# Optimization experiments

Measured on AMD Instinct MI355X. Metric: run time of the kernel, lower is better.

The kernel has to match this reference:

```python
import jax, jax.numpy as jnp
import numpy as np

N_NODES = 100000
N_EDGES = 3200000
N_FEAT = 128
HIDDEN = 16


def gcn_conv(x, W, b, row, col, ew, n):
    """PyG GCNConv: linear -> add self-loops -> sym deg-norm -> scatter-add -> bias."""
    x = x @ W  # [n, out]
    loop = jnp.arange(n)
    row = jnp.concatenate([row, loop])
    col = jnp.concatenate([col, loop])
    ew = jnp.concatenate([ew, jnp.ones((n,), ew.dtype)])  # self-loop weight 1
    deg = jax.ops.segment_sum(ew, col, num_segments=n)  # in-degree by edge weight
    dinv = jnp.where(deg > 0, jax.lax.rsqrt(deg), 0.0)
    norm = dinv[row] * ew * dinv[col]  # [E+n]
    # gather source features, scale, scatter-add at destinations
    out = jax.ops.segment_sum(x[row] * norm[:, None], col, num_segments=n)
    return out + b


def setup_inputs() -> dict:
    key = jax.random.key(0)
    k = jax.random.split(key, 7)
    x = jax.random.normal(k[0], (N_NODES, N_FEAT), dtype=jnp.float32)
    edge_index = jax.random.randint(k[1], (2, N_EDGES), 0, N_NODES, dtype=jnp.int64)
    edge_weight = jax.random.uniform(k[2], (N_EDGES,), dtype=jnp.float32)
    s1 = 1.0 / np.sqrt(N_FEAT)
    s2 = 1.0 / np.sqrt(HIDDEN)
    W1 = jax.random.uniform(k[3], (N_FEAT, HIDDEN), jnp.float32, -s1, s1)
    b1 = jnp.zeros((HIDDEN,), jnp.float32)
    W2 = jax.random.uniform(k[4], (HIDDEN, 1), jnp.float32, -s2, s2)
    b2 = jnp.zeros((1,), jnp.float32)
    return {"x": x, "edge_index": edge_index, "edge_weight": edge_weight,
            "W1": W1, "b1": b1, "W2": W2, "b2": b2}


def reference(x, edge_index, edge_weight, W1, b1, W2, b2):
    n = x.shape[0]
    row, col = edge_index[0], edge_index[1]
    h = gcn_conv(x, W1, b1, row, col, edge_weight, n)
    h = jax.nn.relu(h)
    h = gcn_conv(h, W2, b2, row, col, edge_weight, n)
    return jax.nn.sigmoid(h)[:, 0].astype(jnp.float32)  # squeeze(1)
```

## Files before the change

### kernel.cpp

```cpp
#include <hip/hip_runtime.h>
#include <math.h>

#define NNODES 100000
#define NEDGES 3200000
#define NF 128
#define NH 16
#define SB 192
#define NSB 521
#define NBLK 512
#define EPB (NEDGES / NBLK)
#define CAP2 6912

__device__ __forceinline__ unsigned bf16rne(float f) {
    unsigned u = __float_as_uint(f);
    return (u + 0x7fffu + ((u >> 16) & 1u)) >> 16;
}

__global__ void k_hist(const int* __restrict__ col, unsigned* __restrict__ ghist) {
    __shared__ unsigned h[NSB];
    int t = threadIdx.x, b = blockIdx.x;
    for (int i = t; i < NSB; i += 256) h[i] = 0u;
    __syncthreads();
    const int2* c2 = (const int2*)(col + b * EPB);
    for (int i = t; i < EPB / 2; i += 256) {
        int2 c = c2[i];
        atomicAdd(&h[(unsigned)c.x / SB], 1u);
        atomicAdd(&h[(unsigned)c.y / SB], 1u);
    }
    __syncthreads();
    for (int i = t; i < NSB; i += 256) ghist[(size_t)b * NSB + i] = h[i];
}

__global__ __launch_bounds__(NBLK) void k_scan1(unsigned* __restrict__ ghist,
                                                unsigned* __restrict__ totals) {
    int k = blockIdx.x, t = threadIdx.x;
    __shared__ unsigned s[NBLK];
    unsigned v = ghist[(size_t)t * NSB + k];
    s[t] = v;
    __syncthreads();
    for (int off = 1; off < NBLK; off <<= 1) {
        unsigned x = (t >= off) ? s[t - off] : 0u;
        __syncthreads();
        s[t] += x;
        __syncthreads();
    }
    ghist[(size_t)t * NSB + k] = s[t] - v;
    if (t == NBLK - 1) totals[k] = s[t];
}

__global__ void k_scan2(const unsigned* __restrict__ totals, unsigned* __restrict__ sbase,
                        unsigned* __restrict__ start) {
    int t = threadIdx.x;
    __shared__ unsigned s[256];
    unsigned v[3];
    unsigned p = 0;
#pragma unroll
    for (int j = 0; j < 3; ++j) {
        int i = t * 3 + j;
        v[j] = (i < NSB) ? totals[i] : 0u;
        p += v[j];
    }
    s[t] = p;
    __syncthreads();
    for (int off = 1; off < 256; off <<= 1) {
        unsigned x = (t >= off) ? s[t - off] : 0u;
        __syncthreads();
        s[t] += x;
        __syncthreads();
    }
    unsigned run = s[t] - p;
#pragma unroll
    for (int j = 0; j < 3; ++j) {
        int i = t * 3 + j;
        if (i < NSB) sbase[i] = run;
        run += v[j];
    }
    if (t == 255) { sbase[NSB] = NEDGES; start[NNODES] = NEDGES; }
}

__global__ __launch_bounds__(256) void k_scatB1(
        const int* __restrict__ row, const int* __restrict__ col,
        const float* __restrict__ ew,
        const unsigned* __restrict__ ghist, const unsigned* __restrict__ sbase,
        uint2* __restrict__ spack) {
    __shared__ uint2 stage[EPB];
    __shared__ unsigned short sbArr[EPB];
    __shared__ unsigned lcnt[NSB];
    __shared__ unsigned gdelta[NSB];
    __shared__ unsigned scn[256];
    int t = threadIdx.x, b = blockIdx.x;
    int e0 = b * EPB;
    for (int i = t; i < NSB; i += 256) lcnt[i] = 0u;
    __syncthreads();
    const int2* c2 = (const int2*)(col + e0);
    for (int i = t; i < EPB / 2; i += 256) {
        int2 c = c2[i];
        atomicAdd(&lcnt[(unsigned)c.x / SB], 1u);
        atomicAdd(&lcnt[(unsigned)c.y / SB], 1u);
    }
    __syncthreads();
    unsigned v[3];
    unsigned p = 0;
#pragma unroll
    for (int j = 0; j < 3; ++j) {
        int i = t * 3 + j;
        v[j] = (i < NSB) ? lcnt[i] : 0u;
        p += v[j];
    }
    scn[t] = p;
    __syncthreads();
    for (int off = 1; off < 256; off <<= 1) {
        unsigned x = (t >= off) ? scn[t - off] : 0u;
        __syncthreads();
        scn[t] += x;
        __syncthreads();
    }
    unsigned run = scn[t] - p;
    __syncthreads();
    unsigned lst[3];
#pragma unroll
    for (int j = 0; j < 3; ++j) {
        int i = t * 3 + j;
        if (i < NSB) {
            lst[j] = run;
            gdelta[i] = sbase[i] + ghist[(size_t)b * NSB + i] - run;
        }
        run += v[j];
    }
    __syncthreads();
#pragma unroll
    for (int j = 0; j < 3; ++j) {
        int i = t * 3 + j;
        if (i < NSB) lcnt[i] = lst[j];
    }
    __syncthreads();
    const int2* r2 = (const int2*)(row + e0);
    const float2* w2 = (const float2*)(ew + e0);
    for (int i = t; i < EPB / 2; i += 256) {
        int2 rr = r2[i];
        int2 cc = c2[i];
        float2 ww = w2[i];
        unsigned sb = (unsigned)cc.x / SB;
        unsigned ln = (unsigned)cc.x - sb * SB;
        unsigned pos = atomicAdd(&lcnt[sb], 1u);
        stage[pos] = make_uint2((unsigned)rr.x | (ln << 17), __float_as_uint(ww.x));
        sbArr[pos] = (unsigned short)sb;
        sb = (unsigned)cc.y / SB;
        ln = (unsigned)cc.y - sb * SB;
        pos = atomicAdd(&lcnt[sb], 1u);
        stage[pos] = make_uint2((unsigned)rr.y | (ln << 17), __float_as_uint(ww.y));
        sbArr[pos] = (unsigned short)sb;
    }
    __syncthreads();
    for (int i = t; i < EPB; i += 256)
        spack[i + gdelta[sbArr[i]]] = stage[i];
}

__global__ __launch_bounds__(512) void k_sortB2(uint2* __restrict__ spack,
                                                const unsigned* __restrict__ sbase,
                                                unsigned* __restrict__ start,
                                                float* __restrict__ dinv) {
    __shared__ uint2 ed[CAP2];
    __shared__ unsigned hist[SB];
    __shared__ float wdeg[SB];
    __shared__ unsigned scn[512];
    int k = blockIdx.x, t = threadIdx.x;
    unsigned e0 = sbase[k], e1 = sbase[k + 1];
    int ne = (int)(e1 - e0);
    if (t < SB) { hist[t] = 0u; wdeg[t] = 0.f; }
    __syncthreads();
    for (int i = t; i < ne; i += 512) {
        uint2 p = spack[e0 + i];
        unsigned ln = p.x >> 17;
        atomicAdd(&hist[ln], 1u);
        atomicAdd(&wdeg[ln], __uint_as_float(p.y));
    }
    __syncthreads();
    unsigned v = (t < SB) ? hist[t] : 0u;
    scn[t] = v;
    __syncthreads();
    for (int off = 1; off < 512; off <<= 1) {
        unsigned x = (t >= off) ? scn[t - off] : 0u;
        __syncthreads();
        scn[t] += x;
        __syncthreads();
    }
    unsigned excl = scn[t] - v;
    int g = k * SB + t;
    if (t < SB && g < NNODES) {
        start[g] = e0 + excl;
        dinv[g] = rsqrtf(wdeg[t] + 1.0f);
    }
    __syncthreads();
    if (t < SB) hist[t] = excl;
    __syncthreads();
    for (int i = t; i < ne; i += 512) {
        uint2 p = spack[e0 + i];
        unsigned ln = p.x >> 17;
        unsigned pos = atomicAdd(&hist[ln], 1u);
        ed[pos] = make_uint2(p.x & 0x1FFFF, p.y);
    }
    __syncthreads();
    for (int i = t; i < ne; i += 512)
        spack[e0 + i] = ed[i];
}

__global__ void k_xw1n(const float* __restrict__ x, const float* __restrict__ W1,
                       const float* __restrict__ dinv, unsigned* __restrict__ xwn) {
    __shared__ float w[NF * NH];
    for (int t = threadIdx.x; t < NF * NH; t += blockDim.x) w[t] = W1[t];
    __syncthreads();
    int i = blockIdx.x * blockDim.x + threadIdx.x;
    if (i >= NNODES) return;
    float acc[NH];
#pragma unroll
    for (int f = 0; f < NH; ++f) acc[f] = 0.f;
    const float4* xr = (const float4*)(x + (long long)i * NF);
#pragma unroll 8
    for (int k4 = 0; k4 < NF / 4; ++k4) {
        float4 v = xr[k4];
        const float* wk = &w[k4 * 4 * NH];
#pragma unroll
        for (int f = 0; f < NH; ++f)
            acc[f] += v.x * wk[f] + v.y * wk[NH + f] + v.z * wk[2 * NH + f] + v.w * wk[3 * NH + f];
    }
    float di = dinv[i];
    unsigned u[8];
#pragma unroll
    for (int j = 0; j < 8; ++j)
        u[j] = bf16rne(acc[2 * j] * di) | (bf16rne(acc[2 * j + 1] * di) << 16);
    uint4* o = (uint4*)(xwn + (size_t)i * 8);
    o[0] = make_uint4(u[0], u[1], u[2], u[3]);
    o[1] = make_uint4(u[4], u[5], u[6], u[7]);
}

__global__ __launch_bounds__(256) void k_edge1z(
        const uint2* __restrict__ spack, const unsigned* __restrict__ start,
        const unsigned* __restrict__ xwn, const float* __restrict__ dinv,
        const float* __restrict__ b1, const float* __restrict__ W2,
        float* __restrict__ zn) {
    int t = threadIdx.x;
    int n = blockIdx.x * 4 + (t >> 6);
    int lane = t & 63;
    int fg = lane & 3, e4 = lane >> 2;
    unsigned e0 = start[n], e1 = start[n + 1];
    float ax = 0.f, ay = 0.f, az = 0.f, aw = 0.f;
    for (unsigned e = e0 + e4; e < e1; e += 48) {
        unsigned ea = e + 16, eb = e + 32;
        uint2 p0 = spack[e];
        uint2 p1 = spack[ea];
        uint2 p2 = spack[eb];
        bool va = ea < e1, vb = eb < e1;
        unsigned r0 = p0.x;
        unsigned r1 = p1.x & 0x1FFFFu; r1 = r1 < NNODES ? r1 : NNODES - 1u;
        unsigned r2 = p2.x & 0x1FFFFu; r2 = r2 < NNODES ? r2 : NNODES - 1u;
        float w0 = __uint_as_float(p0.y);
        float w1 = va ? __uint_as_float(p1.y) : 0.f;
        float w2 = vb ? __uint_as_float(p2.y) : 0.f;
        uint2 q0 = *(const uint2*)(xwn + (size_t)r0 * 8 + fg * 2);
        uint2 q1 = *(const uint2*)(xwn + (size_t)r1 * 8 + fg * 2);
        uint2 q2 = *(const uint2*)(xwn + (size_t)r2 * 8 + fg * 2);
        ax += __uint_as_float(q0.x << 16) * w0 + __uint_as_float(q1.x << 16) * w1
            + __uint_as_float(q2.x << 16) * w2;
        ay += __uint_as_float(q0.x & 0xffff0000u) * w0 + __uint_as_float(q1.x & 0xffff0000u) * w1
            + __uint_as_float(q2.x & 0xffff0000u) * w2;
        az += __uint_as_float(q0.y << 16) * w0 + __uint_as_float(q1.y << 16) * w1
            + __uint_as_float(q2.y << 16) * w2;
        aw += __uint_as_float(q0.y & 0xffff0000u) * w0 + __uint_as_float(q1.y & 0xffff0000u) * w1
            + __uint_as_float(q2.y & 0xffff0000u) * w2;
    }
#pragma unroll
    for (int m = 4; m < 64; m <<= 1) {
        ax += __shfl_xor(ax, m);
        ay += __shfl_xor(ay, m);
        az += __shfl_xor(az, m);
        aw += __shfl_xor(aw, m);
    }
    uint2 qs = *(const uint2*)(xwn + (size_t)n * 8 + fg * 2);
    ax += __uint_as_float(qs.x << 16);
    ay += __uint_as_float(qs.x & 0xffff0000u);
    az += __uint_as_float(qs.y << 16);
    aw += __uint_as_float(qs.y & 0xffff0000u);
    float di = dinv[n];
    float4 b4 = ((const float4*)b1)[fg];
    float4 w4 = ((const float4*)W2)[fg];
    float s = fmaxf(di * ax + b4.x, 0.f) * w4.x
            + fmaxf(di * ay + b4.y, 0.f) * w4.y
            + fmaxf(di * az + b4.z, 0.f) * w4.z
            + fmaxf(di * aw + b4.w, 0.f) * w4.w;
    s += __shfl_xor(s, 1);
    s += __shfl_xor(s, 2);
    if (lane == 0) zn[n] = s * di;
}

__global__ __launch_bounds__(256) void k_edge2out(
        const uint2* __restrict__ spack, const unsigned* __restrict__ start,
        const float* __restrict__ zn, const float* __restrict__ dinv,
        const float* __restrict__ b2, float* __restrict__ out) {
    int t = threadIdx.x;
    int n = blockIdx.x * 4 + (t >> 6);
    int lane = t & 63;
    unsigned e0 = start[n], e1 = start[n + 1];
    float acc = 0.f;
    for (unsigned e = e0 + lane; e < e1; e += 64) {
        uint2 p = spack[e];
        acc += zn[p.x] * __uint_as_float(p.y);
    }
#pragma unroll
    for (int m = 1; m < 64; m <<= 1) acc += __shfl_xor(acc, m);
    if (lane == 0) {
        float di = dinv[n];
        float v = di * acc + di * zn[n] + b2[0];
        out[n] = 1.f / (1.f + expf(-v));
    }
}

extern "C" void kernel_launch(void* const* d_in, const int* in_sizes, int n_in,
                              void* d_out, int out_size, void* d_ws, size_t ws_size,
                              hipStream_t stream) {
    const float* x  = (const float*)d_in[0];
    const int* eidx = (const int*)d_in[1];
    const float* ew = (const float*)d_in[2];
    const float* W1 = (const float*)d_in[3];
    const float* b1 = (const float*)d_in[4];
    const float* W2 = (const float*)d_in[5];
    const float* b2 = (const float*)d_in[6];
    float* out = (float*)d_out;

    const int* row = eidx;
    const int* col = eidx + NEDGES;

    unsigned* ws = (unsigned*)d_ws;
    uint2*    spack  = (uint2*)ws;
    unsigned* xwn    = ws + 6400000;
    float*    dinv   = (float*)(ws + 7200000);
    float*    zn     = (float*)(ws + 7300000);
    unsigned* start  = ws + 7400000;
    unsigned* sbase  = ws + 7500001;
    unsigned* totals = ws + 7500523;
    unsigned* ghist  = ws + 7501044;

    k_hist   <<<NBLK, 256, 0, stream>>>(col, ghist);
    k_scan1  <<<NSB, NBLK, 0, stream>>>(ghist, totals);
    k_scan2  <<<1, 256, 0, stream>>>(totals, sbase, start);
    k_scatB1 <<<NBLK, 256, 0, stream>>>(row, col, ew, ghist, sbase, spack);
    k_sortB2 <<<NSB, 512, 0, stream>>>(spack, sbase, start, dinv);
    k_xw1n   <<<(NNODES + 255) / 256, 256, 0, stream>>>(x, W1, dinv, xwn);
    k_edge1z <<<NNODES / 4, 256, 0, stream>>>(spack, start, xwn, dinv, b1, W2, zn);
    k_edge2out<<<NNODES / 4, 256, 0, stream>>>(spack, start, zn, dinv, b2, out);
}
```

Before: 159.4 us.

## Replace per-node CSR sort with per-superblock LDS atomic accumulation

Drops the second-level sort that built per-node CSR offsets. Instead, each of the 521 superblocks accumulates its destination features with shared-memory float atomics, in both the layer-1 and layer-2 aggregations. The x@W1 matmul is folded into the histogram launch as extra blocks writing fp32 xw, and a separate pass applies dinv and converts to bf16. This saves the sort pass and its LDS staging, but costs 16 shared atomics per edge in layer 1, more contention, and only 521 blocks of parallelism for the edge work.

```diff
diff --git a/kernel.cpp b/kernel.cpp
--- a/kernel.cpp
+++ b/kernel.cpp
@@ -9,26 +9,54 @@
 #define NSB 521
 #define NBLK 512
 #define EPB (NEDGES / NBLK)
-#define CAP2 6912
+#define XWBLK 391
 
 __device__ __forceinline__ unsigned bf16rne(float f) {
     unsigned u = __float_as_uint(f);
     return (u + 0x7fffu + ((u >> 16) & 1u)) >> 16;
 }
-
-__global__ void k_hist(const int* __restrict__ col, unsigned* __restrict__ ghist) {
+__device__ __forceinline__ float bflo(unsigned u) { return __uint_as_float(u << 16); }
+__device__ __forceinline__ float bfhi(unsigned u) { return __uint_as_float(u & 0xffff0000u); }
+
+__global__ void k_histxw(const int* __restrict__ col, unsigned* __restrict__ ghist,
+                         const float* __restrict__ x, const float* __restrict__ W1,
+                         float* __restrict__ xw) {
+    __shared__ float w[NF * NH];
     __shared__ unsigned h[NSB];
     int t = threadIdx.x, b = blockIdx.x;
-    for (int i = t; i < NSB; i += 256) h[i] = 0u;
-    __syncthreads();
-    const int2* c2 = (const int2*)(col + b * EPB);
-    for (int i = t; i < EPB / 2; i += 256) {
-        int2 c = c2[i];
-        atomicAdd(&h[(unsigned)c.x / SB], 1u);
-        atomicAdd(&h[(unsigned)c.y / SB], 1u);
-    }
-    __syncthreads();
-    for (int i = t; i < NSB; i += 256) ghist[(size_t)b * NSB + i] = h[i];
+    if (b < NBLK) {
+        for (int i = t; i < NSB; i += 256) h[i] = 0u;
+        __syncthreads();
+        const int2* c2 = (const int2*)(col + b * EPB);
+        for (int i = t; i < EPB / 2; i += 256) {
+            int2 c = c2[i];
+            atomicAdd(&h[(unsigned)c.x / SB], 1u);
+            atomicAdd(&h[(unsigned)c.y / SB], 1u);
+        }
+        __syncthreads();
+        for (int i = t; i < NSB; i += 256) ghist[(size_t)b * NSB + i] = h[i];
+    } else {
+        for (int i = t; i < NF * NH; i += 256) w[i] = W1[i];
+        __syncthreads();
+        int i = (b - NBLK) * 256 + t;
+        if (i >= NNODES) return;
+        float acc[NH];
+#pragma unroll
+        for (int f = 0; f < NH; ++f) acc[f] = 0.f;
+        const float4* xr = (const float4*)(x + (long long)i * NF);
+#pragma unroll 8
+        for (int k4 = 0; k4 < NF / 4; ++k4) {
+            float4 v = xr[k4];
+            const float* wk = &w[k4 * 4 * NH];
+#pragma unroll
+            for (int f = 0; f < NH; ++f)
+                acc[f] += v.x * wk[f] + v.y * wk[NH + f] + v.z * wk[2 * NH + f] + v.w * wk[3 * NH + f];
+        }
+        float4* o = (float4*)(xw + (size_t)i * NH);
+#pragma unroll
+        for (int q = 0; q < 4; ++q)
+            o[q] = make_float4(acc[4 * q], acc[4 * q + 1], acc[4 * q + 2], acc[4 * q + 3]);
+    }
 }
 
 __global__ __launch_bounds__(NBLK) void k_scan1(unsigned* __restrict__ ghist,
@@ -48,8 +76,7 @@
     if (t == NBLK - 1) totals[k] = s[t];
 }
 
-__global__ void k_scan2(const unsigned* __restrict__ totals, unsigned* __restrict__ sbase,
-                        unsigned* __restrict__ start) {
+__global__ void k_scan2(const unsigned* __restrict__ totals, unsigned* __restrict__ sbase) {
     int t = threadIdx.x;
     __shared__ unsigned s[256];
     unsigned v[3];
@@ -75,7 +102,7 @@
         if (i < NSB) sbase[i] = run;
         run += v[j];
     }
-    if (t == 255) { sbase[NSB] = NEDGES; start[NNODES] = NEDGES; }
+    if (t == 255) sbase[NSB] = NEDGES;
 }
 
 __global__ __launch_bounds__(256) void k_scatB1(
@@ -156,162 +183,116 @@
         spack[i + gdelta[sbArr[i]]] = stage[i];
 }
 
-__global__ __launch_bounds__(512) void k_sortB2(uint2* __restrict__ spack,
-                                                const unsigned* __restrict__ sbase,
-                                                unsigned* __restrict__ start,
-                                                float* __restrict__ dinv) {
-    __shared__ uint2 ed[CAP2];
-    __shared__ unsigned hist[SB];
+__global__ __launch_bounds__(512) void k_degdinv(
+        const uint2* __restrict__ spack, const unsigned* __restrict__ sbase,
+        const float* __restrict__ xw, float* __restrict__ dinv,
+        unsigned* __restrict__ xwn) {
     __shared__ float wdeg[SB];
-    __shared__ unsigned scn[512];
     int k = blockIdx.x, t = threadIdx.x;
+    if (t < SB) wdeg[t] = 0.f;
+    __syncthreads();
     unsigned e0 = sbase[k], e1 = sbase[k + 1];
-    int ne = (int)(e1 - e0);
-    if (t < SB) { hist[t] = 0u; wdeg[t] = 0.f; }
-    __syncthreads();
-    for (int i = t; i < ne; i += 512) {
-        uint2 p = spack[e0 + i];
-        unsigned ln = p.x >> 17;
-        atomicAdd(&hist[ln], 1u);
-        atomicAdd(&wdeg[ln], __uint_as_float(p.y));
-    }
-    __syncthreads();
-    unsigned v = (t < SB) ? hist[t] : 0u;
-    scn[t] = v;
-    __syncthreads();
-    for (int off = 1; off < 512; off <<= 1) {
-        unsigned x = (t >= off) ? scn[t - off] : 0u;
-        __syncthreads();
-        scn[t] += x;
-        __syncthreads();
-    }
-    unsigned excl = scn[t] - v;
+    for (unsigned e = e0 + t; e < e1; e += 512) {
+        uint2 p = spack[e];
+        atomicAdd(&wdeg[p.x >> 17], __uint_as_float(p.y));
+    }
+    __syncthreads();
     int g = k * SB + t;
     if (t < SB && g < NNODES) {
-        start[g] = e0 + excl;
-        dinv[g] = rsqrtf(wdeg[t] + 1.0f);
-    }
-    __syncthreads();
-    if (t < SB) hist[t] = excl;
-    __syncthreads();
-    for (int i = t; i < ne; i += 512) {
-        uint2 p = spack[e0 + i];
-        unsigned ln = p.x >> 17;
-        unsigned pos = atomicAdd(&hist[ln], 1u);
-        ed[pos] = make_uint2(p.x & 0x1FFFF, p.y);
-    }
-    __syncthreads();
-    for (int i = t; i < ne; i += 512)
-        spack[e0 + i] = ed[i];
-}
-
-__global__ void k_xw1n(const float* __restrict__ x, const float* __restrict__ W1,
-                       const float* __restrict__ dinv, unsigned* __restrict__ xwn) {
-    __shared__ float w[NF * NH];
-    for (int t = threadIdx.x; t < NF * NH; t += blockDim.x) w[t] = W1[t];
-    __syncthreads();
-    int i = blockIdx.x * blockDim.x + threadIdx.x;
-    if (i >= NNODES) return;
-    float acc[NH];
-#pragma unroll
-    for (int f = 0; f < NH; ++f) acc[f] = 0.f;
-    const float4* xr = (const float4*)(x + (long long)i * NF);
-#pragma unroll 8
-    for (int k4 = 0; k4 < NF / 4; ++k4) {
-        float4 v = xr[k4];
-        const float* wk = &w[k4 * 4 * NH];
-#pragma unroll
-        for (int f = 0; f < NH; ++f)
-            acc[f] += v.x * wk[f] + v.y * wk[NH + f] + v.z * wk[2 * NH + f] + v.w * wk[3 * NH + f];
-    }
-    float di = dinv[i];
-    unsigned u[8];
-#pragma unroll
-    for (int j = 0; j < 8; ++j)
-        u[j] = bf16rne(acc[2 * j] * di) | (bf16rne(acc[2 * j + 1] * di) << 16);
-    uint4* o = (uint4*)(xwn + (size_t)i * 8);
-    o[0] = make_uint4(u[0], u[1], u[2], u[3]);
-    o[1] = make_uint4(u[4], u[5], u[6], u[7]);
-}
-
-__global__ __launch_bounds__(256) void k_edge1z(
-        const uint2* __restrict__ spack, const unsigned* __restrict__ start,
+        float di = rsqrtf(wdeg[t] + 1.0f);
+        dinv[g] = di;
+        const float4* xr = (const float4*)(xw + (size_t)g * NH);
+        float4 A = xr[0], B = xr[1], C = xr[2], D = xr[3];
+        unsigned u0 = bf16rne(A.x * di) | (bf16rne(A.y * di) << 16);
+        unsigned u1 = bf16rne(A.z * di) | (bf16rne(A.w * di) << 16);
+        unsigned u2 = bf16rne(B.x * di) | (bf16rne(B.y * di) << 16);
+        unsigned u3 = bf16rne(B.z * di) | (bf16rne(B.w * di) << 16);
+        unsigned u4 = bf16rne(C.x * di) | (bf16rne(C.y * di) << 16);
+        unsigned u5 = bf16rne(C.z * di) | (bf16rne(C.w * di) << 16);
+        unsigned u6 = bf16rne(D.x * di) | (bf16rne(D.y * di) << 16);
+        unsigned u7 = bf16rne(D.z * di) | (bf16rne(D.w * di) << 16);
+        uint4* o = (uint4*)(xwn + (size_t)g * 8);
+        o[0] = make_uint4(u0, u1, u2, u3);
+        o[1] = make_uint4(u4, u5, u6, u7);
+    }
+}
+
+__global__ __launch_bounds__(512) void k_edge1acc(
+        const uint2* __restrict__ spack, const unsigned* __restrict__ sbase,
         const unsigned* __restrict__ xwn, const float* __restrict__ dinv,
         const float* __restrict__ b1, const float* __restrict__ W2,
         float* __restrict__ zn) {
-    int t = threadIdx.x;
-    int n = blockIdx.x * 4 + (t >> 6);
-    int lane = t & 63;
-    int fg = lane & 3, e4 = lane >> 2;
-    unsigned e0 = start[n], e1 = start[n + 1];
-    float ax = 0.f, ay = 0.f, az = 0.f, aw = 0.f;
-    for (unsigned e = e0 + e4; e < e1; e += 48) {
-        unsigned ea = e + 16, eb = e + 32;
-        uint2 p0 = spack[e];
-        uint2 p1 = spack[ea];
-        uint2 p2 = spack[eb];
-        bool va = ea < e1, vb = eb < e1;
-        unsigned r0 = p0.x;
-        unsigned r1 = p1.x & 0x1FFFFu; r1 = r1 < NNODES ? r1 : NNODES - 1u;
-        unsigned r2 = p2.x & 0x1FFFFu; r2 = r2 < NNODES ? r2 : NNODES - 1u;
-        float w0 = __uint_as_float(p0.y);
-        float w1 = va ? __uint_as_float(p1.y) : 0.f;
-        float w2 = vb ? __uint_as_float(p2.y) : 0.f;
-        uint2 q0 = *(const uint2*)(xwn + (size_t)r0 * 8 + fg * 2);
-        uint2 q1 = *(const uint2*)(xwn + (size_t)r1 * 8 + fg * 2);
-        uint2 q2 = *(const uint2*)(xwn + (size_t)r2 * 8 + fg * 2);
-        ax += __uint_as_float(q0.x << 16) * w0 + __uint_as_float(q1.x << 16) * w1
-            + __uint_as_float(q2.x << 16) * w2;
-        ay += __uint_as_float(q0.x & 0xffff0000u) * w0 + __uint_as_float(q1.x & 0xffff0000u) * w1
-            + __uint_as_float(q2.x & 0xffff0000u) * w2;
-        az += __uint_as_float(q0.y << 16) * w0 + __uint_as_float(q1.y << 16) * w1
-            + __uint_as_float(q2.y << 16) * w2;
-        aw += __uint_as_float(q0.y & 0xffff0000u) * w0 + __uint_as_float(q1.y & 0xffff0000u) * w1
-            + __uint_as_float(q2.y & 0xffff0000u) * w2;
-    }
-#pragma unroll
-    for (int m = 4; m < 64; m <<= 1) {
-        ax += __shfl_xor(ax, m);
-        ay += __shfl_xor(ay, m);
-        az += __shfl_xor(az, m);
-        aw += __shfl_xor(aw, m);
-    }
-    uint2 qs = *(const uint2*)(xwn + (size_t)n * 8 + fg * 2);
-    ax += __uint_as_float(qs.x << 16);
-    ay += __uint_as_float(qs.x & 0xffff0000u);
-    az += __uint_as_float(qs.y << 16);
-    aw += __uint_as_float(qs.y & 0xffff0000u);
-    float di = dinv[n];
-    float4 b4 = ((const float4*)b1)[fg];
-    float4 w4 = ((const float4*)W2)[fg];
-    float s = fmaxf(di * ax + b4.x, 0.f) * w4.x
-            + fmaxf(di * ay + b4.y, 0.f) * w4.y
-            + fmaxf(di * az + b4.z, 0.f) * w4.z
-            + fmaxf(di * aw + b4.w, 0.f) * w4.w;
+    __shared__ float facc[SB * 17];
+    int k = blockIdx.x, t = threadIdx.x;
+    for (int i = t; i < SB * 17; i += 512) facc[i] = 0.f;
+    __syncthreads();
+    unsigned e0 = sbase[k], e1 = sbase[k + 1];
+    for (unsigned e = e0 + t; e < e1; e += 512) {
+        uint2 p = spack[e];
+        unsigned r = p.x & 0x1FFFFu;
+        unsigned ln = p.x >> 17;
+        float w = __uint_as_float(p.y);
+        const uint4* q4 = (const uint4*)(xwn + (size_t)r * 8);
+        uint4 qa = q4[0], qb = q4[1];
+        float* f = &facc[ln * 17];
+        atomicAdd(&f[0],  bflo(qa.x) * w);
+        atomicAdd(&f[1],  bfhi(qa.x) * w);
+        atomicAdd(&f[2],  bflo(qa.y) * w);
+        atomicAdd(&f[3],  bfhi(qa.y) * w);
+        atomicAdd(&f[4],  bflo(qa.z) * w);
+        atomicAdd(&f[5],  bfhi(qa.z) * w);
+        atomicAdd(&f[6],  bflo(qa.w) * w);
+        atomicAdd(&f[7],  bfhi(qa.w) * w);
+        atomicAdd(&f[8],  bflo(qb.x) * w);
+        atomicAdd(&f[9],  bfhi(qb.x) * w);
+        atomicAdd(&f[10], bflo(qb.y) * w);
+        atomicAdd(&f[11], bfhi(qb.y) * w);
+        atomicAdd(&f[12], bflo(qb.z) * w);
+        atomicAdd(&f[13], bfhi(qb.z) * w);
+        atomicAdd(&f[14], bflo(qb.w) * w);
+        atomicAdd(&f[15], bfhi(qb.w) * w);
+    }
+    __syncthreads();
+    int n = t >> 1, half = t & 1;
+    int g = k * SB + n;
+    float s = 0.f, di = 0.f;
+    if (n < SB && g < NNODES) {
+        di = dinv[g];
+        uint4 q = ((const uint4*)(xwn + (size_t)g * 8))[half];
+        const float* fr = &facc[n * 17 + half * 8];
+        int fb = half * 8;
+        s += fmaxf(di * (fr[0] + bflo(q.x)) + b1[fb + 0], 0.f) * W2[fb + 0];
+        s += fmaxf(di * (fr[1] + bfhi(q.x)) + b1[fb + 1], 0.f) * W2[fb + 1];
+        s += fmaxf(di * (fr[2] + bflo(q.y)) + b1[fb + 2], 0.f) * W2[fb + 2];
+        s += fmaxf(di * (fr[3] + bfhi(q.y)) + b1[fb + 3], 0.f) * W2[fb + 3];
+        s += fmaxf(di * (fr[4] + bflo(q.z)) + b1[fb + 4], 0.f) * W2[fb + 4];
+        s += fmaxf(di * (fr[5] + bfhi(q.z)) + b1[fb + 5], 0.f) * W2[fb + 5];
+        s += fmaxf(di * (fr[6] + bflo(q.w)) + b1[fb + 6], 0.f) * W2[fb + 6];
+        s += fmaxf(di * (fr[7] + bfhi(q.w)) + b1[fb + 7], 0.f) * W2[fb + 7];
+    }
     s += __shfl_xor(s, 1);
-    s += __shfl_xor(s, 2);
-    if (lane == 0) zn[n] = s * di;
-}
-
-__global__ __launch_bounds__(256) void k_edge2out(
-        const uint2* __restrict__ spack, const unsigned* __restrict__ start,
+    if (half == 0 && n < SB && g < NNODES) zn[g] = s * di;
+}
+
+__global__ __launch_bounds__(512) void k_edge2acc(
+        const uint2* __restrict__ spack, const unsigned* __restrict__ sbase,
         const float* __restrict__ zn, const float* __restrict__ dinv,
         const float* __restrict__ b2, float* __restrict__ out) {
-    int t = threadIdx.x;
-    int n = blockIdx.x * 4 + (t >> 6);
-    int lane = t & 63;
-    unsigned e0 = start[n], e1 = start[n + 1];
-    float acc = 0.f;
-    for (unsigned e = e0 + lane; e < e1; e += 64) {
+    __shared__ float zacc[SB];
+    int k = blockIdx.x, t = threadIdx.x;
+    if (t < SB) zacc[t] = 0.f;
+    __syncthreads();
+    unsigned e0 = sbase[k], e1 = sbase[k + 1];
+    for (unsigned e = e0 + t; e < e1; e += 512) {
         uint2 p = spack[e];
-        acc += zn[p.x] * __uint_as_float(p.y);
-    }
-#pragma unroll
-    for (int m = 1; m < 64; m <<= 1) acc += __shfl_xor(acc, m);
-    if (lane == 0) {
-        float di = dinv[n];
-        float v = di * acc + di * zn[n] + b2[0];
-        out[n] = 1.f / (1.f + expf(-v));
+        atomicAdd(&zacc[p.x >> 17], zn[p.x & 0x1FFFFu] * __uint_as_float(p.y));
+    }
+    __syncthreads();
+    int g = k * SB + t;
+    if (t < SB && g < NNODES) {
+        float di = dinv[g];
+        float v = di * zacc[t] + di * zn[g] + b2[0];
+        out[g] = 1.f / (1.f + expf(-v));
     }
 }
 
@@ -332,20 +313,19 @@
 
     unsigned* ws = (unsigned*)d_ws;
     uint2*    spack  = (uint2*)ws;
-    unsigned* xwn    = ws + 6400000;
-    float*    dinv   = (float*)(ws + 7200000);
-    float*    zn     = (float*)(ws + 7300000);
-    unsigned* start  = ws + 7400000;
-    unsigned* sbase  = ws + 7500001;
-    unsigned* totals = ws + 7500523;
-    unsigned* ghist  = ws + 7501044;
-
-    k_hist   <<<NBLK, 256, 0, stream>>>(col, ghist);
+    float*    xw     = (float*)(ws + 6400000);
+    unsigned* xwn    = ws + 8000000;
+    float*    dinv   = (float*)(ws + 8800000);
+    float*    zn     = (float*)(ws + 8900000);
+    unsigned* sbase  = ws + 9000000;
+    unsigned* totals = ws + 9000522;
+    unsigned* ghist  = ws + 9001043;
+
+    k_histxw <<<NBLK + XWBLK, 256, 0, stream>>>(col, ghist, x, W1, xw);
     k_scan1  <<<NSB, NBLK, 0, stream>>>(ghist, totals);
-    k_scan2  <<<1, 256, 0, stream>>>(totals, sbase, start);
+    k_scan2  <<<1, 256, 0, stream>>>(totals, sbase);
     k_scatB1 <<<NBLK, 256, 0, stream>>>(row, col, ew, ghist, sbase, spack);
-    k_sortB2 <<<NSB, 512, 0, stream>>>(spack, sbase, start, dinv);
-    k_xw1n   <<<(NNODES + 255) / 256, 256, 0, stream>>>(x, W1, dinv, xwn);
-    k_edge1z <<<NNODES / 4, 256, 0, stream>>>(spack, start, xwn, dinv, b1, W2, zn);
-    k_edge2out<<<NNODES / 4, 256, 0, stream>>>(spack, start, zn, dinv, b2, out);
-}
+    k_degdinv<<<NSB, 512, 0, stream>>>(spack, sbase, xw, dinv, xwn);
+    k_edge1acc<<<NSB, 512, 0, stream>>>(spack, sbase, xwn, dinv, b1, W2, zn);
+    k_edge2acc<<<NSB, 512, 0, stream>>>(spack, sbase, zn, dinv, b2, out);
+}
```

Measured after the change: 479.7 us. 201% more time.

## Fuse X·W1 into histogram kernel and store fp32 features scaled in sort

Applied to the files above, without the earlier changes.

The dense X·W1 projection now runs as extra blocks inside the histogram kernel, so it overlaps the edge histogram and needs one fewer launch. Because dinv is not known yet at that point, the kernel stores unscaled fp32 features, and the sort kernel later rescales each node's row by dinv in place. The bf16 packing is dropped, so the edge gather reads 16-byte fp32 values instead of 8-byte bf16 values. That doubles the gather traffic in the first aggregation and adds a read-modify-write pass over the features.

```diff
diff --git a/kernel.cpp b/kernel.cpp
--- a/kernel.cpp
+++ b/kernel.cpp
@@ -10,25 +10,47 @@
 #define NBLK 512
 #define EPB (NEDGES / NBLK)
 #define CAP2 6912
-
-__device__ __forceinline__ unsigned bf16rne(float f) {
-    unsigned u = __float_as_uint(f);
-    return (u + 0x7fffu + ((u >> 16) & 1u)) >> 16;
-}
-
-__global__ void k_hist(const int* __restrict__ col, unsigned* __restrict__ ghist) {
+#define XWBLK 391
+
+__global__ void k_histxw(const int* __restrict__ col, unsigned* __restrict__ ghist,
+                         const float* __restrict__ x, const float* __restrict__ W1,
+                         float* __restrict__ xw) {
+    __shared__ float w[NF * NH];
     __shared__ unsigned h[NSB];
     int t = threadIdx.x, b = blockIdx.x;
-    for (int i = t; i < NSB; i += 256) h[i] = 0u;
-    __syncthreads();
-    const int2* c2 = (const int2*)(col + b * EPB);
-    for (int i = t; i < EPB / 2; i += 256) {
-        int2 c = c2[i];
-        atomicAdd(&h[(unsigned)c.x / SB], 1u);
-        atomicAdd(&h[(unsigned)c.y / SB], 1u);
-    }
-    __syncthreads();
-    for (int i = t; i < NSB; i += 256) ghist[(size_t)b * NSB + i] = h[i];
+    if (b < NBLK) {
+        for (int i = t; i < NSB; i += 256) h[i] = 0u;
+        __syncthreads();
+        const int2* c2 = (const int2*)(col + b * EPB);
+        for (int i = t; i < EPB / 2; i += 256) {
+            int2 c = c2[i];
+            atomicAdd(&h[(unsigned)c.x / SB], 1u);
+            atomicAdd(&h[(unsigned)c.y / SB], 1u);
+        }
+        __syncthreads();
+        for (int i = t; i < NSB; i += 256) ghist[(size_t)b * NSB + i] = h[i];
+    } else {
+        for (int i = t; i < NF * NH; i += 256) w[i] = W1[i];
+        __syncthreads();
+        int i = (b - NBLK) * 256 + t;
+        if (i >= NNODES) return;
+        float acc[NH];
+#pragma unroll
+        for (int f = 0; f < NH; ++f) acc[f] = 0.f;
+        const float4* xr = (const float4*)(x + (long long)i * NF);
+#pragma unroll 8
+        for (int k4 = 0; k4 < NF / 4; ++k4) {
+            float4 v = xr[k4];
+            const float* wk = &w[k4 * 4 * NH];
+#pragma unroll
+            for (int f = 0; f < NH; ++f)
+                acc[f] += v.x * wk[f] + v.y * wk[NH + f] + v.z * wk[2 * NH + f] + v.w * wk[3 * NH + f];
+        }
+        float4* o = (float4*)(xw + (size_t)i * NH);
+#pragma unroll
+        for (int q = 0; q < 4; ++q)
+            o[q] = make_float4(acc[4 * q], acc[4 * q + 1], acc[4 * q + 2], acc[4 * q + 3]);
+    }
 }
 
 __global__ __launch_bounds__(NBLK) void k_scan1(unsigned* __restrict__ ghist,
@@ -159,7 +181,8 @@
 __global__ __launch_bounds__(512) void k_sortB2(uint2* __restrict__ spack,
                                                 const unsigned* __restrict__ sbase,
                                                 unsigned* __restrict__ start,
-                                                float* __restrict__ dinv) {
+                                                float* __restrict__ dinv,
+                                                float* __restrict__ xw) {
     __shared__ uint2 ed[CAP2];
     __shared__ unsigned hist[SB];
     __shared__ float wdeg[SB];
@@ -187,9 +210,11 @@
     }
     unsigned excl = scn[t] - v;
     int g = k * SB + t;
+    float di = 0.f;
     if (t < SB && g < NNODES) {
         start[g] = e0 + excl;
-        dinv[g] = rsqrtf(wdeg[t] + 1.0f);
+        di = rsqrtf(wdeg[t] + 1.0f);
+        dinv[g] = di;
     }
     __syncthreads();
     if (t < SB) hist[t] = excl;
@@ -203,40 +228,20 @@
     __syncthreads();
     for (int i = t; i < ne; i += 512)
         spack[e0 + i] = ed[i];
-}
-
-__global__ void k_xw1n(const float* __restrict__ x, const float* __restrict__ W1,
-                       const float* __restrict__ dinv, unsigned* __restrict__ xwn) {
-    __shared__ float w[NF * NH];
-    for (int t = threadIdx.x; t < NF * NH; t += blockDim.x) w[t] = W1[t];
-    __syncthreads();
-    int i = blockIdx.x * blockDim.x + threadIdx.x;
-    if (i >= NNODES) return;
-    float acc[NH];
-#pragma unroll
-    for (int f = 0; f < NH; ++f) acc[f] = 0.f;
-    const float4* xr = (const float4*)(x + (long long)i * NF);
-#pragma unroll 8
-    for (int k4 = 0; k4 < NF / 4; ++k4) {
-        float4 v = xr[k4];
-        const float* wk = &w[k4 * 4 * NH];
-#pragma unroll
-        for (int f = 0; f < NH; ++f)
-            acc[f] += v.x * wk[f] + v.y * wk[NH + f] + v.z * wk[2 * NH + f] + v.w * wk[3 * NH + f];
-    }
-    float di = dinv[i];
-    unsigned u[8];
-#pragma unroll
-    for (int j = 0; j < 8; ++j)
-        u[j] = bf16rne(acc[2 * j] * di) | (bf16rne(acc[2 * j + 1] * di) << 16);
-    uint4* o = (uint4*)(xwn + (size_t)i * 8);
-    o[0] = make_uint4(u[0], u[1], u[2], u[3]);
-    o[1] = make_uint4(u[4], u[5], u[6], u[7]);
+    if (t < SB && g < NNODES) {
+        float4* p4 = (float4*)(xw + (size_t)g * NH);
+#pragma unroll
+        for (int q = 0; q < 4; ++q) {
+            float4 vv = p4[q];
+            vv.x *= di; vv.y *= di; vv.z *= di; vv.w *= di;
+            p4[q] = vv;
+        }
+    }
 }
 
 __global__ __launch_bounds__(256) void k_edge1z(
         const uint2* __restrict__ spack, const unsigned* __restrict__ start,
-        const unsigned* __restrict__ xwn, const float* __restrict__ dinv,
+        const float* __restrict__ xw, const float* __restrict__ dinv,
         const float* __restrict__ b1, const float* __restrict__ W2,
         float* __restrict__ zn) {
     int t = threadIdx.x;
@@ -257,17 +262,13 @@
         float w0 = __uint_as_float(p0.y);
         float w1 = va ? __uint_as_float(p1.y) : 0.f;
         float w2 = vb ? __uint_as_float(p2.y) : 0.f;
-        uint2 q0 = *(const uint2*)(xwn + (size_t)r0 * 8 + fg * 2);
-        uint2 q1 = *(const uint2*)(xwn + (size_t)r1 * 8 + fg * 2);
-        uint2 q2 = *(const uint2*)(xwn + (size_t)r2 * 8 + fg * 2);
-        ax += __uint_as_float(q0.x << 16) * w0 + __uint_as_float(q1.x << 16) * w1
-            + __uint_as_float(q2.x << 16) * w2;
-        ay += __uint_as_float(q0.x & 0xffff0000u) * w0 + __uint_as_float(q1.x & 0xffff0000u) * w1
-            + __uint_as_float(q2.x & 0xffff0000u) * w2;
-        az += __uint_as_float(q0.y << 16) * w0 + __uint_as_float(q1.y << 16) * w1
-            + __uint_as_float(q2.y << 16) * w2;
-        aw += __uint_as_float(q0.y & 0xffff0000u) * w0 + __uint_as_float(q1.y & 0xffff0000u) * w1
-            + __uint_as_float(q2.y & 0xffff0000u) * w2;
+        float4 q0 = *(const float4*)(xw + (size_t)r0 * NH + fg * 4);
+        float4 q1 = *(const float4*)(xw + (size_t)r1 * NH + fg * 4);
+        float4 q2 = *(const float4*)(xw + (size_t)r2 * NH + fg * 4);
+        ax += q0.x * w0 + q1.x * w1 + q2.x * w2;
+        ay += q0.y * w0 + q1.y * w1 + q2.y * w2;
+        az += q0.z * w0 + q1.z * w1 + q2.z * w2;
+        aw += q0.w * w0 + q1.w * w1 + q2.w * w2;
     }
 #pragma unroll
     for (int m = 4; m < 64; m <<= 1) {
@@ -276,11 +277,8 @@
         az += __shfl_xor(az, m);
         aw += __shfl_xor(aw, m);
     }
-    uint2 qs = *(const uint2*)(xwn + (size_t)n * 8 + fg * 2);
-    ax += __uint_as_float(qs.x << 16);
-    ay += __uint_as_float(qs.x & 0xffff0000u);
-    az += __uint_as_float(qs.y << 16);
-    aw += __uint_as_float(qs.y & 0xffff0000u);
+    float4 qs = *(const float4*)(xw + (size_t)n * NH + fg * 4);
+    ax += qs.x; ay += qs.y; az += qs.z; aw += qs.w;
     float di = dinv[n];
     float4 b4 = ((const float4*)b1)[fg];
     float4 w4 = ((const float4*)W2)[fg];
@@ -332,20 +330,19 @@
 
     unsigned* ws = (unsigned*)d_ws;
     uint2*    spack  = (uint2*)ws;
-    unsigned* xwn    = ws + 6400000;
-    float*    dinv   = (float*)(ws + 7200000);
-    float*    zn     = (float*)(ws + 7300000);
-    unsigned* start  = ws + 7400000;
-    unsigned* sbase  = ws + 7500001;
-    unsigned* totals = ws + 7500523;
-    unsigned* ghist  = ws + 7501044;
-
-    k_hist   <<<NBLK, 256, 0, stream>>>(col, ghist);
+    float*    xw     = (float*)(ws + 6400000);
+    float*    dinv   = (float*)(ws + 8000000);
+    float*    zn     = (float*)(ws + 8100000);
+    unsigned* start  = ws + 8200000;
+    unsigned* sbase  = ws + 8300001;
+    unsigned* totals = ws + 8300523;
+    unsigned* ghist  = ws + 8301044;
+
+    k_histxw <<<NBLK + XWBLK, 256, 0, stream>>>(col, ghist, x, W1, xw);
     k_scan1  <<<NSB, NBLK, 0, stream>>>(ghist, totals);
     k_scan2  <<<1, 256, 0, stream>>>(totals, sbase, start);
     k_scatB1 <<<NBLK, 256, 0, stream>>>(row, col, ew, ghist, sbase, spack);
-    k_sortB2 <<<NSB, 512, 0, stream>>>(spack, sbase, start, dinv);
-    k_xw1n   <<<(NNODES + 255) / 256, 256, 0, stream>>>(x, W1, dinv, xwn);
-    k_edge1z <<<NNODES / 4, 256, 0, stream>>>(spack, start, xwn, dinv, b1, W2, zn);
+    k_sortB2 <<<NSB, 512, 0, stream>>>(spack, sbase, start, dinv, xw);
+    k_edge1z <<<NNODES / 4, 256, 0, stream>>>(spack, start, xw, dinv, b1, W2, zn);
     k_edge2out<<<NNODES / 4, 256, 0, stream>>>(spack, start, zn, dinv, b2, out);
 }
```

Measured after the change: 154.9 us. -2.8%, faster.
